# Optimization experiments

Measured on AMD Instinct MI355X. Metric: run time of the kernel, lower is better.

Reference implementation:

```python
import jax, jax.numpy as jnp
import numpy as np
from jax import lax

DIM = 10
BATCH = 65536

def setup_inputs() -> dict:
    key = jax.random.key(0)
    ks = jax.random.split(key, 9)
    return {
        "x": jax.random.normal(ks[0], (BATCH, DIM, DIM), dtype=jnp.float32),
        "w1": jax.random.normal(ks[1], (10, 1, 1, 1), dtype=jnp.float32) * 0.3,
        "b1": jax.random.normal(ks[2], (10,), dtype=jnp.float32) * 0.1,
        "w2": jax.random.normal(ks[3], (1, 10, 3, 3), dtype=jnp.float32) * 0.1,
        "b2": jax.random.normal(ks[4], (1,), dtype=jnp.float32) * 0.1,
        "fc1_w": jax.random.normal(ks[5], (4, DIM), dtype=jnp.float32) * 0.3,
        "fc1_b": jax.random.normal(ks[6], (4,), dtype=jnp.float32) * 0.1,
        "fc2_w": jax.random.normal(ks[7], (2, 4), dtype=jnp.float32) * 0.3,
        "fc2_b": jax.random.normal(ks[8], (2,), dtype=jnp.float32) * 0.1,
    }

def reference(x, w1, b1, w2, b2, fc1_w, fc1_b, fc2_w, fc2_b):
    # convEdge: BrainNetCNN edge-to-edge, out[i,j] = row_sum(i) + col_sum(j)
    row = jnp.sum(x, axis=-1, keepdims=True)        # [B, D, 1]
    col = jnp.sum(x, axis=-2, keepdims=True)        # [B, 1, D]
    e2e = (row + col)[:, None, :, :]                # [B, 1, D, D]
    # Conv2d(1, 10, 1) + ReLU: a 1x1 conv is a per-channel scale + bias
    h = jax.nn.relu(e2e * w1[None, :, 0, 0, 0, None, None] + b1[None, :, None, None])  # [B,10,D,D]
    # convSym: lower-triangular mask per channel
    mask = jnp.tril(jnp.ones((DIM, DIM), dtype=h.dtype))
    h = h * mask
    # Conv2d(10, 1, 3, stride=1, padding=1) + ReLU
    h = lax.conv_general_dilated(h, w2, window_strides=(1, 1), padding='SAME',
                                 dimension_numbers=('NCHW', 'OIHW', 'NCHW'))
    h = jax.nn.relu(h + b2[None, :, None, None])    # [B, 1, D, D]
    # convVert: edge-to-vertex, out[i] = row_sum(i) + col_sum(i) of channel 0
    m = h[:, 0]                                     # [B, D, D]
    v = jnp.sum(m, axis=-1) + jnp.sum(m, axis=-2)   # [B, D]
    # fc1 -> relu -> fc2
    v = jax.nn.relu(v @ fc1_w.T + fc1_b)
    return v @ fc2_w.T + fc2_b                      # [B, 2]
```

## Files before the change

### kernel.cpp

```cpp
#include <hip/hip_runtime.h>

#define DIM 10
#define BATCH 65536

typedef _Float16 h2 __attribute__((ext_vector_type(2)));

#if defined(__has_builtin)
#  if __has_builtin(__builtin_amdgcn_fdot2)
#    define HAS_FDOT2 1
#  endif
#endif
#ifndef HAS_FDOT2
#  define HAS_FDOT2 0
#endif

__launch_bounds__(256, 1)
__global__ void net_kernel(const float* __restrict__ x,
                           const float* __restrict__ w1,
                           const float* __restrict__ b1,
                           const float* __restrict__ w2,
                           const float* __restrict__ b2,
                           const float* __restrict__ fc1_w,
                           const float* __restrict__ fc1_b,
                           const float* __restrict__ fc2_w,
                           const float* __restrict__ fc2_b,
                           float* __restrict__ out) {
    __shared__ __align__(16) float xs[256 * DIM * DIM];

    const int tid  = threadIdx.x;
    const int wave = tid >> 6;
    const int lane = tid & 63;
    const size_t blk0 = (size_t)blockIdx.x * 256;

    const float* gbase = x + (blk0 + (size_t)wave * 64) * (DIM * DIM);
    float* lbase = xs + wave * 64 * (DIM * DIM);
    #pragma unroll
    for (int c = 0; c < 25; ++c) {
        __builtin_amdgcn_global_load_lds(
            (const __attribute__((address_space(1))) void*)(gbase + c * 256 + lane * 4),
            (__attribute__((address_space(3))) void*)(lbase + c * 256),
            16, 0, 0);
    }

    h2 W1h[5], B1h[5], W2h[5][9];
    #pragma unroll
    for (int cp = 0; cp < 5; ++cp) {
        W1h[cp][0] = (_Float16)w1[2 * cp];     W1h[cp][1] = (_Float16)w1[2 * cp + 1];
        B1h[cp][0] = (_Float16)b1[2 * cp];     B1h[cp][1] = (_Float16)b1[2 * cp + 1];
        #pragma unroll
        for (int k = 0; k < 9; ++k) {
            W2h[cp][k][0] = (_Float16)w2[(2 * cp) * 9 + k];
            W2h[cp][k][1] = (_Float16)w2[(2 * cp + 1) * 9 + k];
        }
    }
    const float B2 = b2[0];

    asm volatile("s_waitcnt vmcnt(0)" ::: "memory");

    float row[DIM], col[DIM];
    #pragma unroll
    for (int i = 0; i < DIM; ++i) { row[i] = 0.f; col[i] = 0.f; }
    const float4* xb = reinterpret_cast<const float4*>(xs + tid * (DIM * DIM));
    #pragma unroll
    for (int t = 0; t < 25; ++t) {
        const float4 v = xb[t];
        const int e0 = t * 4;
        row[(e0 + 0) / DIM] += v.x; col[(e0 + 0) % DIM] += v.x;
        row[(e0 + 1) / DIM] += v.y; col[(e0 + 1) % DIM] += v.y;
        row[(e0 + 2) / DIM] += v.z; col[(e0 + 2) % DIM] += v.z;
        row[(e0 + 3) / DIM] += v.w; col[(e0 + 3) % DIM] += v.w;
    }

    float acc[DIM][DIM];
    #pragma unroll
    for (int i = 0; i < DIM; ++i)
        #pragma unroll
        for (int j = 0; j < DIM; ++j) acc[i][j] = 0.f;

    const h2 zero_h2 = (h2){(_Float16)0, (_Float16)0};

    #pragma unroll
    for (int p = 0; p < DIM; ++p) {
        #pragma unroll
        for (int q = 0; q <= p; ++q) {
            const float e = row[p] + col[q];
            float s[9];
            #pragma unroll
            for (int k = 0; k < 9; ++k) s[k] = 0.f;
#if HAS_FDOT2
            const _Float16 eh = (_Float16)e;
            const h2 e2 = (h2){eh, eh};
            #pragma unroll
            for (int cp = 0; cp < 5; ++cp) {
                h2 g = __builtin_elementwise_fma(W1h[cp], e2, B1h[cp]);
                g = __builtin_elementwise_max(g, zero_h2);
                #pragma unroll
                for (int k = 0; k < 9; ++k)
                    s[k] = __builtin_amdgcn_fdot2(g, W2h[cp][k], s[k], false);
            }
#else
            #pragma unroll
            for (int cp = 0; cp < 5; ++cp) {
                const float g0 = fmaxf(fmaf((float)W1h[cp][0], e, (float)B1h[cp][0]), 0.f);
                const float g1 = fmaxf(fmaf((float)W1h[cp][1], e, (float)B1h[cp][1]), 0.f);
                #pragma unroll
                for (int k = 0; k < 9; ++k) {
                    s[k] = fmaf(g0, (float)W2h[cp][k][0], s[k]);
                    s[k] = fmaf(g1, (float)W2h[cp][k][1], s[k]);
                }
            }
#endif
            #pragma unroll
            for (int a = 0; a < 3; ++a) {
                const int i = p + 1 - a;
                if (i < 0 || i >= DIM) continue;
                #pragma unroll
                for (int bb = 0; bb < 3; ++bb) {
                    const int j = q + 1 - bb;
                    if (j < 0 || j >= DIM) continue;
                    acc[i][j] += s[a * 3 + bb];
                }
            }
        }
    }

    float vsum[DIM];
    #pragma unroll
    for (int k = 0; k < DIM; ++k) vsum[k] = 0.f;
    #pragma unroll
    for (int i = 0; i < DIM; ++i) {
        #pragma unroll
        for (int j = 0; j < DIM; ++j) {
            const float m = fmaxf(acc[i][j] + B2, 0.f);
            vsum[i] += m;
            vsum[j] += m;
        }
    }

    float hid[4];
    #pragma unroll
    for (int t = 0; t < 4; ++t) {
        float a = fc1_b[t];
        #pragma unroll
        for (int k = 0; k < DIM; ++k) a = fmaf(vsum[k], fc1_w[t * DIM + k], a);
        hid[t] = fmaxf(a, 0.f);
    }
    float o0 = fc2_b[0], o1 = fc2_b[1];
    #pragma unroll
    for (int t = 0; t < 4; ++t) {
        o0 = fmaf(hid[t], fc2_w[t], o0);
        o1 = fmaf(hid[t], fc2_w[4 + t], o1);
    }
    reinterpret_cast<float2*>(out)[blk0 + tid] = make_float2(o0, o1);
}

extern "C" void kernel_launch(void* const* d_in, const int* in_sizes, int n_in,
                              void* d_out, int out_size, void* d_ws, size_t ws_size,
                              hipStream_t stream) {
    const float* x     = (const float*)d_in[0];
    const float* w1    = (const float*)d_in[1];
    const float* b1    = (const float*)d_in[2];
    const float* w2    = (const float*)d_in[3];
    const float* b2    = (const float*)d_in[4];
    const float* fc1_w = (const float*)d_in[5];
    const float* fc1_b = (const float*)d_in[6];
    const float* fc2_w = (const float*)d_in[7];
    const float* fc2_b = (const float*)d_in[8];
    float* out = (float*)d_out;

    const int block = 256;
    const int grid = BATCH / block;
    net_kernel<<<grid, block, 0, stream>>>(x, w1, b1, w2, b2, fc1_w, fc1_b,
                                           fc2_w, fc2_b, out);
}
```

Baseline: 16.05 us.

## Split row/col reduction into separate kernel writing workspace, then conv kernel

```diff
diff --git a/kernel.cpp b/kernel.cpp
--- a/kernel.cpp
+++ b/kernel.cpp
@@ -14,17 +14,183 @@
 #  define HAS_FDOT2 0
 #endif
 
+__launch_bounds__(256, 2)
+__global__ void rc_kernel(const float* __restrict__ x, float* __restrict__ rc) {
+    __shared__ __align__(16) float xs[128 * 100];
+
+    const int tid  = threadIdx.x;
+    const int wave = tid >> 6;
+    const int lane = tid & 63;
+    const int l2   = lane >> 1;
+    const int h    = lane & 1;
+    const size_t blk0 = (size_t)blockIdx.x * 128;
+
+    const float* gsrc = x + (blk0 + (size_t)wave * 32) * 100;
+    float* lbase = xs + wave * 3200;
+    #pragma unroll
+    for (int c = 0; c < 12; ++c) {
+        __builtin_amdgcn_global_load_lds(
+            (const __attribute__((address_space(1))) void*)(gsrc + c * 256 + lane * 4),
+            (__attribute__((address_space(3))) void*)(lbase + c * 256),
+            16, 0, 0);
+    }
+    #pragma unroll
+    for (int c = 0; c < 2; ++c) {
+        __builtin_amdgcn_global_load_lds(
+            (const __attribute__((address_space(1))) void*)(gsrc + 3072 + c * 64 + lane),
+            (__attribute__((address_space(3))) void*)(lbase + 3072 + c * 64),
+            4, 0, 0);
+    }
+    asm volatile("s_waitcnt vmcnt(0)" ::: "memory");
+
+    const float4* eb = reinterpret_cast<const float4*>(lbase + l2 * 100);
+    float row[DIM], col[DIM];
+    #pragma unroll
+    for (int i = 0; i < DIM; ++i) { row[i] = 0.f; col[i] = 0.f; }
+    #pragma unroll
+    for (int t = 0; t < 25; ++t) {
+        const float4 v = eb[t];
+        const int e0 = t * 4;
+        row[(e0 + 0) / DIM] += v.x; col[(e0 + 0) % DIM] += v.x;
+        row[(e0 + 1) / DIM] += v.y; col[(e0 + 1) % DIM] += v.y;
+        row[(e0 + 2) / DIM] += v.z; col[(e0 + 2) % DIM] += v.z;
+        row[(e0 + 3) / DIM] += v.w; col[(e0 + 3) % DIM] += v.w;
+    }
+
+    const size_t eg = blk0 + (size_t)wave * 32 + l2;
+    #pragma unroll
+    for (int i = 0; i < DIM; ++i) {
+        const float v = h ? col[i] : row[i];
+        rc[(size_t)(h * 10 + i) * BATCH + eg] = v;
+    }
+}
+
 __launch_bounds__(256, 1)
-__global__ void net_kernel(const float* __restrict__ x,
-                           const float* __restrict__ w1,
-                           const float* __restrict__ b1,
-                           const float* __restrict__ w2,
-                           const float* __restrict__ b2,
-                           const float* __restrict__ fc1_w,
-                           const float* __restrict__ fc1_b,
-                           const float* __restrict__ fc2_w,
-                           const float* __restrict__ fc2_b,
-                           float* __restrict__ out) {
+__global__ void conv_kernel(const float* __restrict__ rc,
+                            const float* __restrict__ w1,
+                            const float* __restrict__ b1,
+                            const float* __restrict__ w2,
+                            const float* __restrict__ b2,
+                            const float* __restrict__ fc1_w,
+                            const float* __restrict__ fc1_b,
+                            const float* __restrict__ fc2_w,
+                            const float* __restrict__ fc2_b,
+                            float* __restrict__ out) {
+    const size_t e = (size_t)blockIdx.x * 256 + threadIdx.x;
+
+    float row[DIM], col[DIM];
+    #pragma unroll
+    for (int i = 0; i < DIM; ++i) row[i] = rc[(size_t)i * BATCH + e];
+    #pragma unroll
+    for (int j = 0; j < DIM; ++j) col[j] = rc[(size_t)(10 + j) * BATCH + e];
+
+    h2 W1h[5], B1h[5], W2h[5][9];
+    #pragma unroll
+    for (int cp = 0; cp < 5; ++cp) {
+        W1h[cp][0] = (_Float16)w1[2 * cp];     W1h[cp][1] = (_Float16)w1[2 * cp + 1];
+        B1h[cp][0] = (_Float16)b1[2 * cp];     B1h[cp][1] = (_Float16)b1[2 * cp + 1];
+        #pragma unroll
+        for (int k = 0; k < 9; ++k) {
+            W2h[cp][k][0] = (_Float16)w2[(2 * cp) * 9 + k];
+            W2h[cp][k][1] = (_Float16)w2[(2 * cp + 1) * 9 + k];
+        }
+    }
+    const float B2 = b2[0];
+
+    float acc[DIM][DIM];
+    #pragma unroll
+    for (int i = 0; i < DIM; ++i)
+        #pragma unroll
+        for (int j = 0; j < DIM; ++j) acc[i][j] = 0.f;
+
+    const h2 zero_h2 = (h2){(_Float16)0, (_Float16)0};
+
+    #pragma unroll
+    for (int p = 0; p < DIM; ++p) {
+        #pragma unroll
+        for (int q = 0; q <= p; ++q) {
+            const float ev = row[p] + col[q];
+            float s[9];
+            #pragma unroll
+            for (int k = 0; k < 9; ++k) s[k] = 0.f;
+#if HAS_FDOT2
+            const _Float16 eh = (_Float16)ev;
+            const h2 e2 = (h2){eh, eh};
+            #pragma unroll
+            for (int cp = 0; cp < 5; ++cp) {
+                h2 g = __builtin_elementwise_fma(W1h[cp], e2, B1h[cp]);
+                g = __builtin_elementwise_max(g, zero_h2);
+                #pragma unroll
+                for (int k = 0; k < 9; ++k)
+                    s[k] = __builtin_amdgcn_fdot2(g, W2h[cp][k], s[k], false);
+            }
+#else
+            #pragma unroll
+            for (int cp = 0; cp < 5; ++cp) {
+                const float g0 = fmaxf(fmaf((float)W1h[cp][0], ev, (float)B1h[cp][0]), 0.f);
+                const float g1 = fmaxf(fmaf((float)W1h[cp][1], ev, (float)B1h[cp][1]), 0.f);
+                #pragma unroll
+                for (int k = 0; k < 9; ++k) {
+                    s[k] = fmaf(g0, (float)W2h[cp][k][0], s[k]);
+                    s[k] = fmaf(g1, (float)W2h[cp][k][1], s[k]);
+                }
+            }
+#endif
+            #pragma unroll
+            for (int a = 0; a < 3; ++a) {
+                const int i = p + 1 - a;
+                if (i < 0 || i >= DIM) continue;
+                #pragma unroll
+                for (int bb = 0; bb < 3; ++bb) {
+                    const int j = q + 1 - bb;
+                    if (j < 0 || j >= DIM) continue;
+                    acc[i][j] += s[a * 3 + bb];
+                }
+            }
+        }
+    }
+
+    float vsum[DIM];
+    #pragma unroll
+    for (int k = 0; k < DIM; ++k) vsum[k] = 0.f;
+    #pragma unroll
+    for (int i = 0; i < DIM; ++i) {
+        #pragma unroll
+        for (int j = 0; j < DIM; ++j) {
+            const float m = fmaxf(acc[i][j] + B2, 0.f);
+            vsum[i] += m;
+            vsum[j] += m;
+        }
+    }
+
+    float hid[4];
+    #pragma unroll
+    for (int t = 0; t < 4; ++t) {
+        float a = fc1_b[t];
+        #pragma unroll
+        for (int k = 0; k < DIM; ++k) a = fmaf(vsum[k], fc1_w[t * DIM + k], a);
+        hid[t] = fmaxf(a, 0.f);
+    }
+    float o0 = fc2_b[0], o1 = fc2_b[1];
+    #pragma unroll
+    for (int t = 0; t < 4; ++t) {
+        o0 = fmaf(hid[t], fc2_w[t], o0);
+        o1 = fmaf(hid[t], fc2_w[4 + t], o1);
+    }
+    reinterpret_cast<float2*>(out)[e] = make_float2(o0, o1);
+}
+
+__launch_bounds__(256, 1)
+__global__ void fused_kernel(const float* __restrict__ x,
+                             const float* __restrict__ w1,
+                             const float* __restrict__ b1,
+                             const float* __restrict__ w2,
+                             const float* __restrict__ b2,
+                             const float* __restrict__ fc1_w,
+                             const float* __restrict__ fc1_b,
+                             const float* __restrict__ fc2_w,
+                             const float* __restrict__ fc2_b,
+                             float* __restrict__ out) {
     __shared__ __align__(16) float xs[256 * DIM * DIM];
 
     const int tid  = threadIdx.x;
@@ -83,12 +249,12 @@
     for (int p = 0; p < DIM; ++p) {
         #pragma unroll
         for (int q = 0; q <= p; ++q) {
-            const float e = row[p] + col[q];
+            const float ev = row[p] + col[q];
             float s[9];
             #pragma unroll
             for (int k = 0; k < 9; ++k) s[k] = 0.f;
 #if HAS_FDOT2
-            const _Float16 eh = (_Float16)e;
+            const _Float16 eh = (_Float16)ev;
             const h2 e2 = (h2){eh, eh};
             #pragma unroll
             for (int cp = 0; cp < 5; ++cp) {
@@ -101,8 +267,8 @@
 #else
             #pragma unroll
             for (int cp = 0; cp < 5; ++cp) {
-                const float g0 = fmaxf(fmaf((float)W1h[cp][0], e, (float)B1h[cp][0]), 0.f);
-                const float g1 = fmaxf(fmaf((float)W1h[cp][1], e, (float)B1h[cp][1]), 0.f);
+                const float g0 = fmaxf(fmaf((float)W1h[cp][0], ev, (float)B1h[cp][0]), 0.f);
+                const float g1 = fmaxf(fmaf((float)W1h[cp][1], ev, (float)B1h[cp][1]), 0.f);
                 #pragma unroll
                 for (int k = 0; k < 9; ++k) {
                     s[k] = fmaf(g0, (float)W2h[cp][k][0], s[k]);
@@ -168,8 +334,16 @@
     const float* fc2_b = (const float*)d_in[8];
     float* out = (float*)d_out;
 
-    const int block = 256;
-    const int grid = BATCH / block;
-    net_kernel<<<grid, block, 0, stream>>>(x, w1, b1, w2, b2, fc1_w, fc1_b,
-                                           fc2_w, fc2_b, out);
+    const size_t rc_bytes = (size_t)20 * BATCH * sizeof(float);
+    if (ws_size >= rc_bytes) {
+        float* rc = (float*)d_ws;
+        rc_kernel<<<512, 256, 0, stream>>>(x, rc);
+        conv_kernel<<<BATCH / 256, 256, 0, stream>>>(rc, w1, b1, w2, b2,
+                                                     fc1_w, fc1_b, fc2_w, fc2_b,
+                                                     out);
+    } else {
+        fused_kernel<<<BATCH / 256, 256, 0, stream>>>(x, w1, b1, w2, b2,
+                                                      fc1_w, fc1_b, fc2_w, fc2_b,
+                                                      out);
+    }
 }
```

After: 21.73 us. 35.4% more time.
